# Optimization experiments

Hardware: AMD Instinct MI355X
Metric: run time of the kernel (lower is better)

Reference implementation:

```python
import jax, jax.numpy as jnp
import numpy as np

N_DEV, N_CAT, N_APP = 100, 1000, 100000
D = 256
E = 100000

EDGES = [("dev", "app", "ei_dev_app", "ew_dev_app"),
         ("app", "cat", "ei_app_cat", "ew_app_cat"),
         ("app", "app", "ei_app_app", "ew_app_app")]
SIZES = {"dev": N_DEV, "cat": N_CAT, "app": N_APP}


def setup_inputs() -> dict:
    key = jax.random.key(0)
    ks = jax.random.split(key, 32)
    s = 1.0 / np.sqrt(D)
    inp = {
        "x_dev": jax.random.normal(ks[0], (N_DEV, D), jnp.float32),
        "x_cat": jax.random.normal(ks[1], (N_CAT, D), jnp.float32),
        "x_app": jax.random.normal(ks[2], (N_APP, D), jnp.float32),
        "ei_dev_app": jnp.stack([jax.random.randint(ks[3], (E,), 0, N_DEV),
                                 jax.random.randint(ks[4], (E,), 0, N_APP)]).astype(jnp.int32),
        "ei_app_cat": jnp.stack([jax.random.randint(ks[5], (E,), 0, N_APP),
                                 jax.random.randint(ks[6], (E,), 0, N_CAT)]).astype(jnp.int32),
        "ei_app_app": jnp.stack([jax.random.randint(ks[7], (E,), 0, N_APP),
                                 jax.random.randint(ks[8], (E,), 0, N_APP)]).astype(jnp.int32),
        "ew_dev_app": jax.random.uniform(ks[9], (E,), jnp.float32, 0.5, 2.0),
        "ew_app_cat": jax.random.uniform(ks[10], (E,), jnp.float32, 0.5, 2.0),
        "ew_app_app": jax.random.uniform(ks[11], (E,), jnp.float32, 0.5, 2.0),
    }
    # per-node-type linear params for layer1 and layer2 (torch nn.Linear equivalents)
    i = 12
    for layer in (1, 2):
        for t in ("dev", "cat", "app"):
            inp[f"W{layer}_{t}"] = jax.random.normal(ks[i], (D, D), jnp.float32) * s
            inp[f"b{layer}_{t}"] = jax.random.normal(ks[i + 1], (D,), jnp.float32) * s
            i += 2
    return inp


def _mp_layer(x, params, ei, ew):
    """One MyMessagePassing layer: per-src-type linear+relu, edge-weighted
    gather, scatter-add into destination node type."""
    # src-type transform (same math as doing it per edge-type iteration)
    h = {t: jax.nn.relu(x[t] @ params[t][0] + params[t][1]) for t in x}
    out = {t: jnp.zeros((SIZES[t], D), x[t].dtype) for t in x}
    for src, dst, ei_name, ew_name in EDGES:
        idx = ei[ei_name]
        msg = h[src][idx[0]] * ew[ew_name][:, None]  # [E, D]
        out[dst] = out[dst] + jax.ops.segment_sum(msg, idx[1], num_segments=SIZES[dst])
    return out


def reference(x_dev, x_cat, x_app,
              ei_dev_app, ei_app_cat, ei_app_app,
              ew_dev_app, ew_app_cat, ew_app_app,
              W1_dev, b1_dev, W1_cat, b1_cat, W1_app, b1_app,
              W2_dev, b2_dev, W2_cat, b2_cat, W2_app, b2_app):
    ei = {"ei_dev_app": ei_dev_app, "ei_app_cat": ei_app_cat, "ei_app_app": ei_app_app}
    ew = {"ew_dev_app": ew_dev_app, "ew_app_cat": ew_app_cat, "ew_app_app": ew_app_app}
    x = {"dev": x_dev, "cat": x_cat, "app": x_app}
    p1 = {"dev": (W1_dev, b1_dev), "cat": (W1_cat, b1_cat), "app": (W1_app, b1_app)}
    p2 = {"dev": (W2_dev, b2_dev), "cat": (W2_cat, b2_cat), "app": (W2_app, b2_app)}
    x = _mp_layer(x, p1, ei, ew)
    x = _mp_layer(x, p2, ei, ew)
    return (x["dev"], x["cat"], x["app"])
```

## Files before the change

### kernel.cpp

```cpp
#include <hip/hip_runtime.h>
#include <cstdint>
#include <cstddef>

#define DD 256
constexpr int NDEV = 100;
constexpr int NCAT = 1000;
constexpr int NAPP = 100000;
constexpr int NE   = 100000;
constexpr int NCNT = NAPP + NAPP + NCAT;

typedef __attribute__((ext_vector_type(8))) short  bf16x8;
typedef __attribute__((ext_vector_type(8))) unsigned short ushort8;
typedef __attribute__((ext_vector_type(4))) float  f32x4;

__device__ __forceinline__ unsigned short f2bf(float f) {
    unsigned int u = __float_as_uint(f);
    u += 0x7fffu + ((u >> 16) & 1u);
    return (unsigned short)(u >> 16);
}
__device__ __forceinline__ float bf2f(unsigned short h) {
    return __uint_as_float((unsigned int)h << 16);
}

__global__ __launch_bounds__(256)
void wsplit_kernel(const float* __restrict__ W, unsigned short* __restrict__ hi,
                   unsigned short* __restrict__ lo) {
    const int idx = blockIdx.x * 256 + threadIdx.x;
    const int k = idx >> 8, n = idx & 255;
    const float f = W[idx];
    const unsigned short h = f2bf(f);
    hi[n * 256 + k] = h;
    lo[n * 256 + k] = f2bf(f - bf2f(h));
}

__global__ __launch_bounds__(256, 3)
void linear_relu_mfma_kernel(const float* __restrict__ A,
                             const unsigned short* __restrict__ Wt_hi,
                             const unsigned short* __restrict__ Wt_lo,
                             const float* __restrict__ bias,
                             float* __restrict__ C, int M) {
    __shared__ unsigned short As_hi[4096];
    __shared__ unsigned short As_lo[4096];

    const int t    = threadIdx.x;
    const int wid  = t >> 6;
    const int lane = t & 63;
    const int wr   = wid >> 1;
    const int wc   = wid & 1;
    const int cl   = lane & 15;
    const int kg   = lane >> 4;
    const int m0   = blockIdx.x * 128;
    const int nb   = blockIdx.y * 128 + wc * 64;

    const int loff = kg * 128 + cl * 8;

    const int sr = t >> 1;
    const int sk = (t & 1) * 16;
    const bool arow_ok = (m0 + sr) < M;
    const float* ap = A + (size_t)(m0 + sr) * DD + sk;
    const int wbase = (sr >> 4) * 512 + (sr & 15) * 8;
    const int kgw   = (sk >> 3);

    f32x4 acc[4][4];
#pragma unroll
    for (int m = 0; m < 4; ++m)
#pragma unroll
        for (int n = 0; n < 4; ++n) acc[m][n] = (f32x4){0.f, 0.f, 0.f, 0.f};

    float pf[16];
#define LOADT(K0)                                                       \
    do {                                                                \
        if (arow_ok) {                                                  \
            _Pragma("unroll")                                           \
            for (int i = 0; i < 4; ++i) {                               \
                const float4 v = *(const float4*)(ap + (K0) + i * 4);   \
                pf[i * 4 + 0] = v.x; pf[i * 4 + 1] = v.y;               \
                pf[i * 4 + 2] = v.z; pf[i * 4 + 3] = v.w;               \
            }                                                           \
        } else {                                                        \
            _Pragma("unroll")                                           \
            for (int i = 0; i < 16; ++i) pf[i] = 0.f;                   \
        }                                                               \
    } while (0)

#define WRITET()                                                        \
    do {                                                                \
        _Pragma("unroll")                                               \
        for (int g = 0; g < 2; ++g) {                                   \
            ushort8 hh, ll;                                             \
            _Pragma("unroll")                                           \
            for (int j = 0; j < 8; ++j) {                               \
                const float f = pf[g * 8 + j];                          \
                const unsigned short h = f2bf(f);                       \
                hh[j] = h;                                              \
                ll[j] = f2bf(f - bf2f(h));                              \
            }                                                           \
            *(ushort8*)&As_hi[wbase + (kgw + g) * 128] = hh;            \
            *(ushort8*)&As_lo[wbase + (kgw + g) * 128] = ll;            \
        }                                                               \
    } while (0)

    LOADT(0);
    WRITET();
    __syncthreads();

    for (int it = 0; it < 8; ++it) {
        const int k0 = it * 32;
        if (it < 7) LOADT(k0 + 32);

        bf16x8 ah[4], al[4], bh[4], bl[4];
#pragma unroll
        for (int m = 0; m < 4; ++m) {
            ah[m] = *(const bf16x8*)&As_hi[(wr * 4 + m) * 512 + loff];
            al[m] = *(const bf16x8*)&As_lo[(wr * 4 + m) * 512 + loff];
        }
#pragma unroll
        for (int n = 0; n < 4; ++n) {
            const size_t wo = (size_t)(nb + n * 16 + cl) * DD + k0 + kg * 8;
            bh[n] = *(const bf16x8*)(Wt_hi + wo);
            bl[n] = *(const bf16x8*)(Wt_lo + wo);
        }
#pragma unroll
        for (int m = 0; m < 4; ++m)
#pragma unroll
            for (int n = 0; n < 4; ++n)
                acc[m][n] = __builtin_amdgcn_mfma_f32_16x16x32_bf16(
                    ah[m], bh[n], acc[m][n], 0, 0, 0);
#pragma unroll
        for (int m = 0; m < 4; ++m)
#pragma unroll
            for (int n = 0; n < 4; ++n)
                acc[m][n] = __builtin_amdgcn_mfma_f32_16x16x32_bf16(
                    al[m], bh[n], acc[m][n], 0, 0, 0);
#pragma unroll
        for (int m = 0; m < 4; ++m)
#pragma unroll
            for (int n = 0; n < 4; ++n)
                acc[m][n] = __builtin_amdgcn_mfma_f32_16x16x32_bf16(
                    ah[m], bl[n], acc[m][n], 0, 0, 0);

        __syncthreads();
        if (it < 7) {
            WRITET();
            __syncthreads();
        }
    }
#undef LOADT
#undef WRITET

    const int r4 = kg << 2;
#pragma unroll
    for (int n = 0; n < 4; ++n) {
        const int col = nb + n * 16 + cl;
        const float bv = bias[col];
#pragma unroll
        for (int m = 0; m < 4; ++m) {
            const int rowb = m0 + wr * 64 + m * 16 + r4;
            float* cp = C + (size_t)rowb * DD + col;
#pragma unroll
            for (int j = 0; j < 4; ++j)
                if (rowb + j < M) cp[(size_t)j * DD] = fmaxf(acc[m][n][j] + bv, 0.f);
        }
    }
}

__global__ __launch_bounds__(256)
void linear_relu_kernel(const float* __restrict__ A, const float* __restrict__ W,
                        const float* __restrict__ bias, float* __restrict__ C,
                        int M) {
    __shared__ float As[8][128];
    __shared__ float Bs[8][128];

    const int t  = threadIdx.x;
    const int m0 = blockIdx.x * 128;
    const int n0 = blockIdx.y * 128;
    const int ra = (t >> 4) << 2;
    const int ca = (t & 15) << 2;

    float acc[8][8];
#pragma unroll
    for (int i = 0; i < 8; ++i)
#pragma unroll
        for (int j = 0; j < 8; ++j) acc[i][j] = 0.f;

    for (int k0 = 0; k0 < DD; k0 += 8) {
        {
            const int row = t >> 1;
            const int kk  = (t & 1) << 2;
            float4 v = make_float4(0.f, 0.f, 0.f, 0.f);
            if (m0 + row < M)
                v = *(const float4*)(A + (size_t)(m0 + row) * DD + k0 + kk);
            As[kk + 0][row] = v.x;
            As[kk + 1][row] = v.y;
            As[kk + 2][row] = v.z;
            As[kk + 3][row] = v.w;
        }
        {
            const int kk = t >> 5;
            const int nn = (t & 31) << 2;
            *(float4*)&Bs[kk][nn] =
                *(const float4*)(W + (size_t)(k0 + kk) * DD + n0 + nn);
        }
        __syncthreads();
#pragma unroll
        for (int k = 0; k < 8; ++k) {
            const float4 a0 = *(const float4*)&As[k][ra];
            const float4 a1 = *(const float4*)&As[k][ra + 64];
            const float4 b0 = *(const float4*)&Bs[k][ca];
            const float4 b1 = *(const float4*)&Bs[k][ca + 64];
            const float av[8] = {a0.x, a0.y, a0.z, a0.w, a1.x, a1.y, a1.z, a1.w};
            const float bv[8] = {b0.x, b0.y, b0.z, b0.w, b1.x, b1.y, b1.z, b1.w};
#pragma unroll
            for (int i = 0; i < 8; ++i)
#pragma unroll
                for (int j = 0; j < 8; ++j)
                    acc[i][j] = fmaf(av[i], bv[j], acc[i][j]);
        }
        __syncthreads();
    }

    const float4 bias0 = *(const float4*)(bias + n0 + ca);
    const float4 bias1 = *(const float4*)(bias + n0 + ca + 64);
#pragma unroll
    for (int i = 0; i < 8; ++i) {
        const int row = m0 + ((i < 4) ? (ra + i) : (ra + 64 + i - 4));
        if (row >= M) continue;
        float4 o0, o1;
        o0.x = fmaxf(acc[i][0] + bias0.x, 0.f);
        o0.y = fmaxf(acc[i][1] + bias0.y, 0.f);
        o0.z = fmaxf(acc[i][2] + bias0.z, 0.f);
        o0.w = fmaxf(acc[i][3] + bias0.w, 0.f);
        o1.x = fmaxf(acc[i][4] + bias1.x, 0.f);
        o1.y = fmaxf(acc[i][5] + bias1.y, 0.f);
        o1.z = fmaxf(acc[i][6] + bias1.z, 0.f);
        o1.w = fmaxf(acc[i][7] + bias1.w, 0.f);
        *(float4*)(C + (size_t)row * DD + n0 + ca)      = o0;
        *(float4*)(C + (size_t)row * DD + n0 + ca + 64) = o1;
    }
}

__global__ __launch_bounds__(256)
void hist3_kernel(const int* __restrict__ d_aa, const int* __restrict__ d_da,
                  const int* __restrict__ d_ac, int* __restrict__ counts) {
    const int g = blockIdx.x * 256 + threadIdx.x;
    if (g < NE)            atomicAdd(&counts[d_aa[g]], 1);
    else if (g < 2 * NE)   atomicAdd(&counts[NAPP + d_da[g - NE]], 1);
    else if (g < 3 * NE)   atomicAdd(&counts[2 * NAPP + d_ac[g - 2 * NE]], 1);
}

__global__ __launch_bounds__(256)
void scan_partial_kernel(const int* __restrict__ counts, int* __restrict__ bsum,
                         int n) {
    __shared__ int sd[256];
    const int t   = threadIdx.x;
    const int idx = blockIdx.x * 1024 + t * 4;
    int s = 0;
    if (idx + 3 < n) {
        const int4 c = *(const int4*)(counts + idx);
        s = c.x + c.y + c.z + c.w;
    } else {
        for (int j = 0; j < 4; ++j) if (idx + j < n) s += counts[idx + j];
    }
    sd[t] = s;
    __syncthreads();
    for (int off = 128; off > 0; off >>= 1) {
        if (t < off) sd[t] += sd[t + off];
        __syncthreads();
    }
    if (t == 0) bsum[blockIdx.x] = sd[0];
}

__global__ __launch_bounds__(256)
void scan_bsum_kernel(const int* __restrict__ bsum, int* __restrict__ boff, int nb) {
    __shared__ int sd[256];
    const int t = threadIdx.x;
    const int v = (t < nb) ? bsum[t] : 0;
    sd[t] = v;
    __syncthreads();
    for (int off = 1; off < 256; off <<= 1) {
        const int w = (t >= off) ? sd[t - off] : 0;
        __syncthreads();
        sd[t] += w;
        __syncthreads();
    }
    if (t < nb) boff[t] = sd[t] - v;
}

__global__ __launch_bounds__(256)
void scan_apply_kernel(int* __restrict__ counts, const int* __restrict__ boff,
                       int* __restrict__ rs, int n) {
    __shared__ int sd[256];
    const int t   = threadIdx.x;
    const int idx = blockIdx.x * 1024 + t * 4;
    int c[4] = {0, 0, 0, 0};
    if (idx + 3 < n) {
        const int4 v = *(const int4*)(counts + idx);
        c[0] = v.x; c[1] = v.y; c[2] = v.z; c[3] = v.w;
    } else {
        for (int j = 0; j < 4; ++j) if (idx + j < n) c[j] = counts[idx + j];
    }
    const int s = c[0] + c[1] + c[2] + c[3];
    sd[t] = s;
    __syncthreads();
    for (int off = 1; off < 256; off <<= 1) {
        const int w = (t >= off) ? sd[t - off] : 0;
        __syncthreads();
        sd[t] += w;
        __syncthreads();
    }
    int o = boff[blockIdx.x] + sd[t] - s;
#pragma unroll
    for (int j = 0; j < 4; ++j) {
        const int i = idx + j;
        if (i < n) {
            rs[i]     = o;
            counts[i] = o;
            o += c[j];
            if (i == n - 1) rs[n] = o;
        }
    }
}

__global__ __launch_bounds__(256)
void fill3_kernel(const int* __restrict__ ei_aa, const float* __restrict__ ew_aa,
                  const int* __restrict__ ei_da, const float* __restrict__ ew_da,
                  const int* __restrict__ ei_ac, const float* __restrict__ ew_ac,
                  int* __restrict__ cursor, int* __restrict__ srcs,
                  float* __restrict__ wsorted) {
    const int g = blockIdx.x * 256 + threadIdx.x;
    if (g >= 3 * NE) return;
    const int*   ei;
    const float* ew;
    int e, base;
    if (g < NE)            { ei = ei_aa; ew = ew_aa; e = g;          base = 0; }
    else if (g < 2 * NE)   { ei = ei_da; ew = ew_da; e = g - NE;     base = NAPP; }
    else                   { ei = ei_ac; ew = ew_ac; e = g - 2 * NE; base = 2 * NAPP; }
    const int d   = ei[NE + e];
    const int pos = atomicAdd(&cursor[base + d], 1);
    srcs[pos]    = ei[e];
    wsorted[pos] = ew[e];
}

__global__ __launch_bounds__(256)
void gather_l1_app_kernel(const float* __restrict__ hA, const float* __restrict__ hD,
                          const int* __restrict__ rsA, const int* __restrict__ rsD,
                          const int* __restrict__ s, const float* __restrict__ w,
                          float* __restrict__ out, int ndst) {
    const int d    = (int)((blockIdx.x * 256 + threadIdx.x) >> 6);
    const int lane = threadIdx.x & 63;
    if (d >= ndst) return;
    const int o = lane << 2;
    float4 acc = make_float4(0.f, 0.f, 0.f, 0.f);
    for (int p = rsA[d], pe = rsA[d + 1]; p < pe; ++p) {
        const float  ww = w[p];
        const float4 v  = *(const float4*)(hA + (size_t)s[p] * DD + o);
        acc.x = fmaf(ww, v.x, acc.x);
        acc.y = fmaf(ww, v.y, acc.y);
        acc.z = fmaf(ww, v.z, acc.z);
        acc.w = fmaf(ww, v.w, acc.w);
    }
    for (int p = rsD[d], pe = rsD[d + 1]; p < pe; ++p) {
        const float  ww = w[p];
        const float4 v  = *(const float4*)(hD + (size_t)s[p] * DD + o);
        acc.x = fmaf(ww, v.x, acc.x);
        acc.y = fmaf(ww, v.y, acc.y);
        acc.z = fmaf(ww, v.z, acc.z);
        acc.w = fmaf(ww, v.w, acc.w);
    }
    *(float4*)(out + (size_t)d * DD + o) = acc;
}

__global__ __launch_bounds__(256)
void gather_l2_app_kernel(const float* __restrict__ hA,
                          const int* __restrict__ rsA, const int* __restrict__ rsD,
                          const int* __restrict__ s, const float* __restrict__ w,
                          const float* __restrict__ b2dev,
                          float* __restrict__ out, int ndst) {
    const int d    = (int)((blockIdx.x * 256 + threadIdx.x) >> 6);
    const int lane = threadIdx.x & 63;
    if (d >= ndst) return;
    const int o = lane << 2;
    float4 acc = make_float4(0.f, 0.f, 0.f, 0.f);
    for (int p = rsA[d], pe = rsA[d + 1]; p < pe; ++p) {
        const float  ww = w[p];
        const float4 v  = *(const float4*)(hA + (size_t)s[p] * DD + o);
        acc.x = fmaf(ww, v.x, acc.x);
        acc.y = fmaf(ww, v.y, acc.y);
        acc.z = fmaf(ww, v.z, acc.z);
        acc.w = fmaf(ww, v.w, acc.w);
    }
    float wsum = 0.f;
    for (int p = rsD[d], pe = rsD[d + 1]; p < pe; ++p) wsum += w[p];
    const float4 b = *(const float4*)(b2dev + o);
    acc.x = fmaf(wsum, fmaxf(b.x, 0.f), acc.x);
    acc.y = fmaf(wsum, fmaxf(b.y, 0.f), acc.y);
    acc.z = fmaf(wsum, fmaxf(b.z, 0.f), acc.z);
    acc.w = fmaf(wsum, fmaxf(b.w, 0.f), acc.w);
    *(float4*)(out + (size_t)d * DD + o) = acc;
}

__global__ __launch_bounds__(256)
void gather_cat_kernel(const float* __restrict__ hA,
                       const int* __restrict__ rs, const int* __restrict__ s,
                       const float* __restrict__ w,
                       float* __restrict__ out, int ndst) {
    const int d    = (int)((blockIdx.x * 256 + threadIdx.x) >> 6);
    const int lane = threadIdx.x & 63;
    if (d >= ndst) return;
    const int o = lane << 2;
    float4 acc = make_float4(0.f, 0.f, 0.f, 0.f);
    for (int p = rs[d], pe = rs[d + 1]; p < pe; ++p) {
        const float  ww = w[p];
        const float4 v  = *(const float4*)(hA + (size_t)s[p] * DD + o);
        acc.x = fmaf(ww, v.x, acc.x);
        acc.y = fmaf(ww, v.y, acc.y);
        acc.z = fmaf(ww, v.z, acc.z);
        acc.w = fmaf(ww, v.w, acc.w);
    }
    *(float4*)(out + (size_t)d * DD + o) = acc;
}

extern "C" void kernel_launch(void* const* d_in, const int* in_sizes, int n_in,
                              void* d_out, int out_size, void* d_ws, size_t ws_size,
                              hipStream_t stream) {
    const float* x_dev  = (const float*)d_in[0];
    const float* x_app  = (const float*)d_in[2];
    const int*   ei_da  = (const int*)d_in[3];
    const int*   ei_ac  = (const int*)d_in[4];
    const int*   ei_aa  = (const int*)d_in[5];
    const float* ew_da  = (const float*)d_in[6];
    const float* ew_ac  = (const float*)d_in[7];
    const float* ew_aa  = (const float*)d_in[8];
    const float* W1_dev = (const float*)d_in[9];
    const float* b1_dev = (const float*)d_in[10];
    const float* W1_app = (const float*)d_in[13];
    const float* b1_app = (const float*)d_in[14];
    const float* b2_dev = (const float*)d_in[16];
    const float* W2_app = (const float*)d_in[19];
    const float* b2_app = (const float*)d_in[20];

    float* out     = (float*)d_out;
    float* out_cat = out + (size_t)NDEV * DD;
    float* out_app = out + (size_t)(NDEV + NCAT) * DD;

    float* h_app  = (float*)d_ws;
    float* h_dev  = h_app + (size_t)NAPP * DD;
    int*   counts = (int*)(h_dev + (size_t)NDEV * DD);
    int*   rs_all = counts + NCNT;
    int*   s_all  = rs_all + NCNT + 1;
    float* w_all  = (float*)(s_all + 3 * NE);
    int*   bsum   = (int*)(w_all + 3 * NE);
    int*   boff   = bsum + 256;

    int* rs_aa = rs_all;
    int* rs_da = rs_all + NAPP;
    int* rs_ac = rs_all + 2 * NAPP;

    unsigned short* wt1_hi = (unsigned short*)counts;
    unsigned short* wt1_lo = wt1_hi + 65536;
    unsigned short* wt2_hi = wt1_lo + 65536;
    unsigned short* wt2_lo = wt2_hi + 65536;

    const int  nblk = (NCNT + 1023) / 1024;
    const dim3 gMfma((NAPP + 127) / 128, 2);
    const int  gGatherApp = (NAPP + 3) / 4;
    const int  gGatherCat = (NCAT + 3) / 4;
    const int  g3e = (3 * NE + 255) / 256;

    hipMemsetAsync(counts, 0, (size_t)NCNT * sizeof(int), stream);
    hist3_kernel<<<g3e, 256, 0, stream>>>(ei_aa + NE, ei_da + NE, ei_ac + NE, counts);
    scan_partial_kernel<<<nblk, 256, 0, stream>>>(counts, bsum, NCNT);
    scan_bsum_kernel<<<1, 256, 0, stream>>>(bsum, boff, nblk);
    scan_apply_kernel<<<nblk, 256, 0, stream>>>(counts, boff, rs_all, NCNT);
    fill3_kernel<<<g3e, 256, 0, stream>>>(ei_aa, ew_aa, ei_da, ew_da, ei_ac, ew_ac,
                                          counts, s_all, w_all);

    wsplit_kernel<<<256, 256, 0, stream>>>(W1_app, wt1_hi, wt1_lo);
    wsplit_kernel<<<256, 256, 0, stream>>>(W2_app, wt2_hi, wt2_lo);

    linear_relu_mfma_kernel<<<gMfma, 256, 0, stream>>>(x_app, wt1_hi, wt1_lo,
                                                       b1_app, h_app, NAPP);
    linear_relu_kernel<<<dim3(1, 2), 256, 0, stream>>>(x_dev, W1_dev, b1_dev,
                                                       h_dev, NDEV);
    gather_l1_app_kernel<<<gGatherApp, 256, 0, stream>>>(
        h_app, h_dev, rs_aa, rs_da, s_all, w_all, out_app, NAPP);

    linear_relu_mfma_kernel<<<gMfma, 256, 0, stream>>>(out_app, wt2_hi, wt2_lo,
                                                       b2_app, h_app, NAPP);
    gather_l2_app_kernel<<<gGatherApp, 256, 0, stream>>>(
        h_app, rs_aa, rs_da, s_all, w_all, b2_dev, out_app, NAPP);
    gather_cat_kernel<<<gGatherCat, 256, 0, stream>>>(
        h_app, rs_ac, s_all, w_all, out_cat, NCAT);

    hipMemsetAsync(out, 0, (size_t)NDEV * DD * sizeof(float), stream);
}
```

Measured before the change: 656.5 us.

## Pre-split activations to bf16 hi/lo and stage GEMM A tiles via direct global-to-LDS loads

Activations are converted to bf16 hi/lo planes once, in a separate split kernel for layer 1 and fused into the layer-1 gather epilogue for layer 2. The GEMM then loads A with global_load_lds into a double-buffered, XOR-swizzled LDS tile instead of loading fp32 and converting in registers. The epilogue is also rewritten to go through LDS so output stores are coalesced float4 writes. This removes in-loop conversion work and one barrier per k-step, at the cost of an extra split kernel pass and reuse of the output buffer as scratch for the bf16 planes.

```diff
diff --git a/kernel.cpp b/kernel.cpp
--- a/kernel.cpp
+++ b/kernel.cpp
@@ -11,6 +11,7 @@
 
 typedef __attribute__((ext_vector_type(8))) short  bf16x8;
 typedef __attribute__((ext_vector_type(8))) unsigned short ushort8;
+typedef __attribute__((ext_vector_type(4))) unsigned short ushort4v;
 typedef __attribute__((ext_vector_type(4))) float  f32x4;
 
 __device__ __forceinline__ unsigned short f2bf(float f) {
@@ -33,14 +34,32 @@
     lo[n * 256 + k] = f2bf(f - bf2f(h));
 }
 
+__global__ __launch_bounds__(256)
+void asplit_kernel(const float* __restrict__ X, unsigned short* __restrict__ hi,
+                   unsigned short* __restrict__ lo) {
+    const size_t base = ((size_t)blockIdx.x * 256 + threadIdx.x) * 8;
+    const float4 v0 = *(const float4*)(X + base);
+    const float4 v1 = *(const float4*)(X + base + 4);
+    const float fv[8] = {v0.x, v0.y, v0.z, v0.w, v1.x, v1.y, v1.z, v1.w};
+    ushort8 hh, ll;
+#pragma unroll
+    for (int j = 0; j < 8; ++j) {
+        const unsigned short h = f2bf(fv[j]);
+        hh[j] = h;
+        ll[j] = f2bf(fv[j] - bf2f(h));
+    }
+    *(ushort8*)(hi + base) = hh;
+    *(ushort8*)(lo + base) = ll;
+}
+
 __global__ __launch_bounds__(256, 3)
-void linear_relu_mfma_kernel(const float* __restrict__ A,
-                             const unsigned short* __restrict__ Wt_hi,
-                             const unsigned short* __restrict__ Wt_lo,
-                             const float* __restrict__ bias,
-                             float* __restrict__ C, int M) {
-    __shared__ unsigned short As_hi[4096];
-    __shared__ unsigned short As_lo[4096];
+void gemm_bf16pair_kernel(const unsigned short* __restrict__ Ahi,
+                          const unsigned short* __restrict__ Alo,
+                          const unsigned short* __restrict__ Wt_hi,
+                          const unsigned short* __restrict__ Wt_lo,
+                          const float* __restrict__ bias,
+                          float* __restrict__ C, int M) {
+    __shared__ alignas(16) unsigned char lds[32768];
 
     const int t    = threadIdx.x;
     const int wid  = t >> 6;
@@ -52,14 +71,27 @@
     const int m0   = blockIdx.x * 128;
     const int nb   = blockIdx.y * 128 + wc * 64;
 
-    const int loff = kg * 128 + cl * 8;
-
-    const int sr = t >> 1;
-    const int sk = (t & 1) * 16;
-    const bool arow_ok = (m0 + sr) < M;
-    const float* ap = A + (size_t)(m0 + sr) * DD + sk;
-    const int wbase = (sr >> 4) * 512 + (sr & 15) * 8;
-    const int kgw   = (sk >> 3);
+    const int s_half   = wid >> 1;
+    const int s_plane  = wid & 1;
+    const int s_rowl   = lane >> 2;
+    const int s_kgslot = lane & 3;
+    const unsigned short* Ap = s_plane ? Alo : Ahi;
+    const int s_kgsrc = s_kgslot ^ ((s_rowl >> 1) & 3);
+
+#define STAGE(BUF, K0)                                                        \
+    do {                                                                      \
+        _Pragma("unroll")                                                     \
+        for (int j = 0; j < 4; ++j) {                                         \
+            const int row  = s_half * 64 + j * 16 + s_rowl;                   \
+            const int rowg = min(m0 + row, M - 1);                            \
+            const unsigned char* src = (const unsigned char*)Ap               \
+                + (size_t)rowg * 512 + (size_t)(K0) * 2 + s_kgsrc * 16;       \
+            unsigned char* dst = lds + (BUF) * 16384 + s_plane * 8192         \
+                                 + (s_half * 64 + j * 16) * 64;               \
+            __builtin_amdgcn_global_load_lds((const unsigned int*)src,        \
+                                             (unsigned int*)dst, 16, 0, 0);   \
+        }                                                                     \
+    } while (0)
 
     f32x4 acc[4][4];
 #pragma unroll
@@ -67,58 +99,30 @@
 #pragma unroll
         for (int n = 0; n < 4; ++n) acc[m][n] = (f32x4){0.f, 0.f, 0.f, 0.f};
 
-    float pf[16];
-#define LOADT(K0)                                                       \
-    do {                                                                \
-        if (arow_ok) {                                                  \
-            _Pragma("unroll")                                           \
-            for (int i = 0; i < 4; ++i) {                               \
-                const float4 v = *(const float4*)(ap + (K0) + i * 4);   \
-                pf[i * 4 + 0] = v.x; pf[i * 4 + 1] = v.y;               \
-                pf[i * 4 + 2] = v.z; pf[i * 4 + 3] = v.w;               \
-            }                                                           \
-        } else {                                                        \
-            _Pragma("unroll")                                           \
-            for (int i = 0; i < 16; ++i) pf[i] = 0.f;                   \
-        }                                                               \
-    } while (0)
-
-#define WRITET()                                                        \
-    do {                                                                \
-        _Pragma("unroll")                                               \
-        for (int g = 0; g < 2; ++g) {                                   \
-            ushort8 hh, ll;                                             \
-            _Pragma("unroll")                                           \
-            for (int j = 0; j < 8; ++j) {                               \
-                const float f = pf[g * 8 + j];                          \
-                const unsigned short h = f2bf(f);                       \
-                hh[j] = h;                                              \
-                ll[j] = f2bf(f - bf2f(h));                              \
-            }                                                           \
-            *(ushort8*)&As_hi[wbase + (kgw + g) * 128] = hh;            \
-            *(ushort8*)&As_lo[wbase + (kgw + g) * 128] = ll;            \
-        }                                                               \
-    } while (0)
-
-    LOADT(0);
-    WRITET();
+    const int kg_eff = kg ^ ((cl >> 1) & 3);
+
+    STAGE(0, 0);
     __syncthreads();
 
+    int cur = 0;
     for (int it = 0; it < 8; ++it) {
         const int k0 = it * 32;
-        if (it < 7) LOADT(k0 + 32);
-
-        bf16x8 ah[4], al[4], bh[4], bl[4];
-#pragma unroll
-        for (int m = 0; m < 4; ++m) {
-            ah[m] = *(const bf16x8*)&As_hi[(wr * 4 + m) * 512 + loff];
-            al[m] = *(const bf16x8*)&As_lo[(wr * 4 + m) * 512 + loff];
-        }
+        bf16x8 bh[4], bl[4];
 #pragma unroll
         for (int n = 0; n < 4; ++n) {
-            const size_t wo = (size_t)(nb + n * 16 + cl) * DD + k0 + kg * 8;
+            const size_t wo = (size_t)(nb + n * 16 + cl) * 256 + k0 + kg * 8;
             bh[n] = *(const bf16x8*)(Wt_hi + wo);
             bl[n] = *(const bf16x8*)(Wt_lo + wo);
+        }
+        if (it < 7) STAGE(cur ^ 1, k0 + 32);
+
+        bf16x8 ah[4], al[4];
+#pragma unroll
+        for (int m = 0; m < 4; ++m) {
+            const int lrow = wr * 64 + m * 16 + cl;
+            const int off  = cur * 16384 + lrow * 64 + kg_eff * 16;
+            ah[m] = *(const bf16x8*)(lds + off);
+            al[m] = *(const bf16x8*)(lds + off + 8192);
         }
 #pragma unroll
         for (int m = 0; m < 4; ++m)
@@ -140,26 +144,30 @@
                     ah[m], bl[n], acc[m][n], 0, 0, 0);
 
         __syncthreads();
-        if (it < 7) {
-            WRITET();
-            __syncthreads();
-        }
-    }
-#undef LOADT
-#undef WRITET
-
-    const int r4 = kg << 2;
-#pragma unroll
-    for (int n = 0; n < 4; ++n) {
-        const int col = nb + n * 16 + cl;
-        const float bv = bias[col];
-#pragma unroll
-        for (int m = 0; m < 4; ++m) {
-            const int rowb = m0 + wr * 64 + m * 16 + r4;
-            float* cp = C + (size_t)rowb * DD + col;
+        cur ^= 1;
+    }
+#undef STAGE
+
+    float* scr = (float*)lds + wid * 1088;
+    const int er2 = lane >> 4;
+    const int ec2 = (lane & 15) * 4;
+#pragma unroll
+    for (int m = 0; m < 4; ++m) {
+#pragma unroll
+        for (int n = 0; n < 4; ++n) {
+            const float bv = bias[nb + n * 16 + cl];
 #pragma unroll
             for (int j = 0; j < 4; ++j)
-                if (rowb + j < M) cp[(size_t)j * DD] = fmaxf(acc[m][n][j] + bv, 0.f);
+                scr[(kg * 4 + j) * 68 + n * 16 + cl] =
+                    fmaxf(acc[m][n][j] + bv, 0.f);
+        }
+#pragma unroll
+        for (int q = 0; q < 4; ++q) {
+            const int row  = q * 4 + er2;
+            const int rowC = m0 + wr * 64 + m * 16 + row;
+            const float4 v = *(const float4*)&scr[row * 68 + ec2];
+            if (rowC < M)
+                *(float4*)(C + (size_t)rowC * DD + nb + ec2) = v;
         }
     }
 }
@@ -342,10 +350,11 @@
 }
 
 __global__ __launch_bounds__(256)
-void gather_l1_app_kernel(const float* __restrict__ hA, const float* __restrict__ hD,
-                          const int* __restrict__ rsA, const int* __restrict__ rsD,
-                          const int* __restrict__ s, const float* __restrict__ w,
-                          float* __restrict__ out, int ndst) {
+void gather_l1_split_kernel(const float* __restrict__ hA, const float* __restrict__ hD,
+                            const int* __restrict__ rsA, const int* __restrict__ rsD,
+                            const int* __restrict__ s, const float* __restrict__ w,
+                            unsigned short* __restrict__ outh,
+                            unsigned short* __restrict__ outl, int ndst) {
     const int d    = (int)((blockIdx.x * 256 + threadIdx.x) >> 6);
     const int lane = threadIdx.x & 63;
     if (d >= ndst) return;
@@ -367,7 +376,17 @@
         acc.z = fmaf(ww, v.z, acc.z);
         acc.w = fmaf(ww, v.w, acc.w);
     }
-    *(float4*)(out + (size_t)d * DD + o) = acc;
+    const float fv[4] = {acc.x, acc.y, acc.z, acc.w};
+    ushort4v hh, ll;
+#pragma unroll
+    for (int j = 0; j < 4; ++j) {
+        const unsigned short h = f2bf(fv[j]);
+        hh[j] = h;
+        ll[j] = f2bf(fv[j] - bf2f(h));
+    }
+    const size_t ob = (size_t)d * DD + o;
+    *(ushort4v*)(outh + ob) = hh;
+    *(ushort4v*)(outl + ob) = ll;
 }
 
 __global__ __launch_bounds__(256)
@@ -443,6 +462,9 @@
     float* out_cat = out + (size_t)NDEV * DD;
     float* out_app = out + (size_t)(NDEV + NCAT) * DD;
 
+    unsigned short* aph = (unsigned short*)out_app;
+    unsigned short* apl = aph + (size_t)NAPP * DD;
+
     float* h_app  = (float*)d_ws;
     float* h_dev  = h_app + (size_t)NAPP * DD;
     int*   counts = (int*)(h_dev + (size_t)NDEV * DD);
@@ -466,6 +488,7 @@
     const int  gGatherApp = (NAPP + 3) / 4;
     const int  gGatherCat = (NCAT + 3) / 4;
     const int  g3e = (3 * NE + 255) / 256;
+    const int  gSplit = (NAPP * DD / 8) / 256;
 
     hipMemsetAsync(counts, 0, (size_t)NCNT * sizeof(int), stream);
     hist3_kernel<<<g3e, 256, 0, stream>>>(ei_aa + NE, ei_da + NE, ei_ac + NE, counts);
@@ -478,15 +501,16 @@
     wsplit_kernel<<<256, 256, 0, stream>>>(W1_app, wt1_hi, wt1_lo);
     wsplit_kernel<<<256, 256, 0, stream>>>(W2_app, wt2_hi, wt2_lo);
 
-    linear_relu_mfma_kernel<<<gMfma, 256, 0, stream>>>(x_app, wt1_hi, wt1_lo,
-                                                       b1_app, h_app, NAPP);
+    asplit_kernel<<<gSplit, 256, 0, stream>>>(x_app, aph, apl);
+    gemm_bf16pair_kernel<<<gMfma, 256, 0, stream>>>(aph, apl, wt1_hi, wt1_lo,
+                                                    b1_app, h_app, NAPP);
     linear_relu_kernel<<<dim3(1, 2), 256, 0, stream>>>(x_dev, W1_dev, b1_dev,
                                                        h_dev, NDEV);
-    gather_l1_app_kernel<<<gGatherApp, 256, 0, stream>>>(
-        h_app, h_dev, rs_aa, rs_da, s_all, w_all, out_app, NAPP);
-
-    linear_relu_mfma_kernel<<<gMfma, 256, 0, stream>>>(out_app, wt2_hi, wt2_lo,
-                                                       b2_app, h_app, NAPP);
+    gather_l1_split_kernel<<<gGatherApp, 256, 0, stream>>>(
+        h_app, h_dev, rs_aa, rs_da, s_all, w_all, aph, apl, NAPP);
+
+    gemm_bf16pair_kernel<<<gMfma, 256, 0, stream>>>(aph, apl, wt2_hi, wt2_lo,
+                                                    b2_app, h_app, NAPP);
     gather_l2_app_kernel<<<gGatherApp, 256, 0, stream>>>(
         h_app, rs_aa, rs_da, s_all, w_all, b2_dev, out_app, NAPP);
     gather_cat_kernel<<<gGatherCat, 256, 0, stream>>>(
```

New measurement: 657.4 us. Within noise of the previous version (+0.1%).
